# Performance work log

Measured on AMD Instinct MI355X. Metric: run time of the kernel, lower is better.

Reference implementation:

```python
import jax, jax.numpy as jnp
import numpy as np

EMBED_DIM = 1024
NUM_HEADS = 16
HEAD_DIM = EMBED_DIM // NUM_HEADS
B, N = 4, 2048


def setup_inputs() -> dict:
    key = jax.random.key(0)
    k = jax.random.split(key, 5)
    scale = 1.0 / np.sqrt(EMBED_DIM)
    return {
        "x": jax.random.normal(k[0], (B, N, EMBED_DIM), dtype=jnp.float32),
        # torch nn.Linear convention: y = x @ W.T + b, W shape [out, in]
        "qkv_w": jax.random.uniform(k[1], (3 * EMBED_DIM, EMBED_DIM), jnp.float32, -scale, scale),
        "qkv_b": jax.random.uniform(k[2], (3 * EMBED_DIM,), jnp.float32, -scale, scale),
        "out_w": jax.random.uniform(k[3], (EMBED_DIM, EMBED_DIM), jnp.float32, -scale, scale),
        "out_b": jax.random.uniform(k[4], (EMBED_DIM,), jnp.float32, -scale, scale),
    }


def reference(x, qkv_w, qkv_b, out_w, out_b):
    b, n, e = x.shape
    qkv = x @ qkv_w.T + qkv_b                      # [B,N,3E]
    qkv = qkv.reshape(b, n, 3, NUM_HEADS, HEAD_DIM)
    qkv = jnp.transpose(qkv, (2, 0, 3, 1, 4))      # [3,B,H,N,D]
    q, k, v = qkv[0], qkv[1], qkv[2]
    scores = jnp.einsum("bhqd,bhkd->bhqk", q, k) / np.sqrt(HEAD_DIM)
    weights = jax.nn.softmax(scores, axis=-1)
    attn = jnp.einsum("bhqk,bhkd->bhqd", weights, v)  # [B,H,N,D]
    attn = jnp.transpose(attn, (0, 2, 1, 3)).reshape(b, n, e)
    return attn @ out_w.T + out_b
```

## Files before the change

### kernel.cpp

```cpp
#include <hip/hip_runtime.h>
#include <hip/hip_bf16.h>

#define EMBED 1024
#define NHEADS 16
#define HDIM 64
#define BATCH 4
#define SEQ 2048
#define MROWS (BATCH*SEQ)
#define QKVN (3*EMBED)
#define KDIM 1024

typedef __bf16 bf16;
typedef __bf16 bf16x4 __attribute__((ext_vector_type(4)));
typedef __bf16 bf16x8 __attribute__((ext_vector_type(8)));
typedef float f32x4 __attribute__((ext_vector_type(4)));
typedef float f32x16 __attribute__((ext_vector_type(16)));

#define QSCALE 0.18033688011112042f

#define NX (MROWS*EMBED/4)
#define NQ (QKVN*KDIM/4)
#define NO (EMBED*KDIM/4)
__global__ void cvt_all(const float* __restrict__ x, const float* __restrict__ qw,
                        const float* __restrict__ ow,
                        bf16* __restrict__ xb, bf16* __restrict__ qwb, bf16* __restrict__ owb) {
    int i = blockIdx.x * blockDim.x + threadIdx.x;
    const float* src; bf16* dst; int j;
    if (i < NX)            { src = x;  dst = xb;  j = i; }
    else if (i < NX + NQ)  { src = qw; dst = qwb; j = i - NX; }
    else if (i < NX+NQ+NO) { src = ow; dst = owb; j = i - NX - NQ; }
    else return;
    float4 f = ((const float4*)src)[j];
    bf16x4 o;
    o[0] = (bf16)f.x; o[1] = (bf16)f.y; o[2] = (bf16)f.z; o[3] = (bf16)f.w;
    *((bf16x4*)dst + j) = o;
}

template<int MODE>
__launch_bounds__(256)
__global__ void gemm_bt(const bf16* __restrict__ A, const bf16* __restrict__ B,
                        const float* __restrict__ bias,
                        float* __restrict__ outF,
                        bf16* __restrict__ Qb, bf16* __restrict__ Kb, bf16* __restrict__ Vt)
{
    __shared__ __align__(16) char ldsmem[16384];
    bf16 (*Alds)[32] = (bf16(*)[32])ldsmem;
    bf16 (*Blds)[32] = (bf16(*)[32])(ldsmem + 8192);
    bf16* bounce = (bf16*)ldsmem;

    const int tid = threadIdx.x;
    const int l = tid & 63, w = tid >> 6;
    const int wr = w >> 1, wc = w & 1;
    const int tM = blockIdx.y * 128, tN = blockIdx.x * 128;

    f32x4 acc[4][4] = {};
    const bf16* Abase = A + (size_t)tM * KDIM;
    const bf16* Bbase = B + (size_t)tN * KDIM;

    for (int k0 = 0; k0 < KDIM; k0 += 32) {
        #pragma unroll
        for (int t = 0; t < 2; ++t) {
            int idx = t * 256 + tid;
            int row = idx >> 2;
            int kc = (idx & 3) * 8;
            __builtin_amdgcn_global_load_lds(
                (const __attribute__((address_space(1))) void*)(Abase + (size_t)row * KDIM + k0 + kc),
                (__attribute__((address_space(3))) void*)((char*)&Alds[0][0] + idx * 16),
                16, 0, 0);
            __builtin_amdgcn_global_load_lds(
                (const __attribute__((address_space(1))) void*)(Bbase + (size_t)row * KDIM + k0 + kc),
                (__attribute__((address_space(3))) void*)((char*)&Blds[0][0] + idx * 16),
                16, 0, 0);
        }
        __syncthreads();
        bf16x8 a[4], b[4];
        #pragma unroll
        for (int i = 0; i < 4; ++i)
            a[i] = *(const bf16x8*)&Alds[wr * 64 + i * 16 + (l & 15)][(l >> 4) * 8];
        #pragma unroll
        for (int j = 0; j < 4; ++j)
            b[j] = *(const bf16x8*)&Blds[wc * 64 + j * 16 + (l & 15)][(l >> 4) * 8];
        #pragma unroll
        for (int i = 0; i < 4; ++i)
            #pragma unroll
            for (int j = 0; j < 4; ++j)
                acc[i][j] = __builtin_amdgcn_mfma_f32_16x16x32_bf16(a[i], b[j], acc[i][j], 0, 0, 0);
        __syncthreads();
    }

    if (MODE == 1) {
        #pragma unroll
        for (int i = 0; i < 4; ++i) {
            #pragma unroll
            for (int j = 0; j < 4; ++j) {
                int n = tN + wc * 64 + j * 16 + (l & 15);
                float bv = bias[n];
                #pragma unroll
                for (int r = 0; r < 4; ++r) {
                    int m = tM + wr * 64 + i * 16 + (l >> 4) * 4 + r;
                    outF[(size_t)m * EMBED + n] = acc[i][j][r] + bv;
                }
            }
        }
    } else {
        const int which = tN >> 10;
        const int bidx  = tM >> 11;
        const int hd0   = (tN & 1023) >> 6;
        const int t32base = (tM & 2047) >> 5;
        bf16* dstbase = (which == 0) ? Qb : (which == 1) ? Kb : Vt;
        const float scale = (which == 0) ? QSCALE : 1.0f;

        float bj[4];
        #pragma unroll
        for (int j = 0; j < 4; ++j)
            bj[j] = bias[tN + wc * 64 + j * 16 + (l & 15)];

        #pragma unroll
        for (int pass = 0; pass < 2; ++pass) {
            __syncthreads();
            #pragma unroll
            for (int ii = 0; ii < 2; ++ii) {
                const int i = pass * 2 + ii;
                #pragma unroll
                for (int j = 0; j < 4; ++j) {
                    const int d = (wc * 64 + j * 16 + (l & 15)) & 63;
                    #pragma unroll
                    for (int r = 0; r < 4; ++r) {
                        const int nsl = wr * 64 + i * 16 + (l >> 4) * 4 + r;
                        float v = acc[i][j][r] + bj[j];
                        int off;
                        if (which == 2) {
                            int dblk = d >> 5;
                            int rem16 = nsl & 15;
                            int c = (nsl >> 4) & 1;
                            int fj = (rem16 & 3) | ((rem16 & 8) >> 1);
                            int fhi = (rem16 >> 2) & 1;
                            int lane = (d & 31) | (fhi << 5);
                            off = (dblk * 2 + c) * 512 + lane * 8 + fj;
                        } else {
                            int kk = d >> 4, fhi = (d >> 3) & 1, fj = d & 7;
                            int lane = (nsl & 31) | (fhi << 5);
                            off = kk * 512 + lane * 8 + fj;
                        }
                        bounce[(wc * 2 + wr) * 2048 + off] = (bf16)(v * scale);
                    }
                }
            }
            __syncthreads();
            const int chunk = tid >> 6;
            size_t gbase = ((size_t)(bidx * NHEADS + hd0 + (chunk >> 1)) * 64
                            + t32base + 2 * (chunk & 1) + pass) * 2048;
            #pragma unroll
            for (int s = 0; s < 4; ++s) {
                int eoff = s * 512 + (tid & 63) * 8;
                *(bf16x8*)(dstbase + gbase + eoff) = *(const bf16x8*)&bounce[chunk * 2048 + eoff];
            }
        }
    }
}

__launch_bounds__(256)
__global__ void gemm_bt64(const bf16* __restrict__ A, const bf16* __restrict__ B,
                          const float* __restrict__ bias, float* __restrict__ outF)
{
    __shared__ bf16 Alds[64][32];
    __shared__ bf16 Blds[128][32];
    const int tid = threadIdx.x;
    const int l = tid & 63, w = tid >> 6;
    const int tM = blockIdx.y * 64, tN = blockIdx.x * 128;

    f32x4 acc[4][2] = {};
    const bf16* Abase = A + (size_t)tM * KDIM;
    const bf16* Bbase = B + (size_t)tN * KDIM;

    for (int k0 = 0; k0 < KDIM; k0 += 32) {
        {
            int row = tid >> 2;
            int kc = (tid & 3) * 8;
            __builtin_amdgcn_global_load_lds(
                (const __attribute__((address_space(1))) void*)(Abase + (size_t)row * KDIM + k0 + kc),
                (__attribute__((address_space(3))) void*)((char*)&Alds[0][0] + tid * 16),
                16, 0, 0);
        }
        #pragma unroll
        for (int t = 0; t < 2; ++t) {
            int idx = t * 256 + tid;
            int row = idx >> 2;
            int kc = (idx & 3) * 8;
            __builtin_amdgcn_global_load_lds(
                (const __attribute__((address_space(1))) void*)(Bbase + (size_t)row * KDIM + k0 + kc),
                (__attribute__((address_space(3))) void*)((char*)&Blds[0][0] + idx * 16),
                16, 0, 0);
        }
        __syncthreads();
        bf16x8 a[4], b[2];
        #pragma unroll
        for (int i = 0; i < 4; ++i)
            a[i] = *(const bf16x8*)&Alds[i * 16 + (l & 15)][(l >> 4) * 8];
        #pragma unroll
        for (int j = 0; j < 2; ++j)
            b[j] = *(const bf16x8*)&Blds[w * 32 + j * 16 + (l & 15)][(l >> 4) * 8];
        #pragma unroll
        for (int i = 0; i < 4; ++i)
            #pragma unroll
            for (int j = 0; j < 2; ++j)
                acc[i][j] = __builtin_amdgcn_mfma_f32_16x16x32_bf16(a[i], b[j], acc[i][j], 0, 0, 0);
        __syncthreads();
    }

    #pragma unroll
    for (int i = 0; i < 4; ++i) {
        #pragma unroll
        for (int j = 0; j < 2; ++j) {
            int n = tN + w * 32 + j * 16 + (l & 15);
            float bv = bias[n];
            #pragma unroll
            for (int r = 0; r < 4; ++r) {
                int m = tM + i * 16 + (l >> 4) * 4 + r;
                outF[(size_t)m * EMBED + n] = acc[i][j][r] + bv;
            }
        }
    }
}

static __device__ __forceinline__ unsigned cvt_pk(float lo, float hi) {
    unsigned r;
    asm("v_cvt_pk_bf16_f32 %0, %1, %2" : "=v"(r) : "v"(lo), "v"(hi));
    return r;
}

__launch_bounds__(256)
__global__ void attn_kernel(const bf16* __restrict__ Qb, const bf16* __restrict__ Kb,
                            const bf16* __restrict__ Vt, bf16* __restrict__ AO)
{
    const int tid = threadIdx.x, l = tid & 63, w = tid >> 6;
    const int lo5 = l & 31, hi = l >> 5;
    int bid = blockIdx.x;
    int swz = (bid & 7) * 128 + (bid >> 3);
    const int bh = swz >> 4;
    const int qt = swz & 15;

    const bf16* QFh = Qb + (size_t)bh * (64 * 2048);
    const bf16* Kit = Kb + (size_t)bh * (64 * 2048) + (size_t)l * 8;
    const bf16* Vit = Vt + (size_t)bh * (64 * 2048) + (size_t)l * 8;

    const int qtile = qt * 4 + w;
    const bf16* qbase = QFh + (size_t)qtile * 2048 + (size_t)l * 8;
    bf16x8 qf[4];
    #pragma unroll
    for (int kk = 0; kk < 4; ++kk)
        qf[kk] = *(const bf16x8*)(qbase + kk * 512);

    f32x16 O0 = {}, O1 = {};
    float lsum = 0.f;
    const f32x16 ZR = {};

    bf16x8 kK0 = *(const bf16x8*)(Kit);
    bf16x8 kK1 = *(const bf16x8*)(Kit + 512);
    bf16x8 kK2 = *(const bf16x8*)(Kit + 1024);
    bf16x8 kK3 = *(const bf16x8*)(Kit + 1536);
    f32x16 SA, SB;
    SA = __builtin_amdgcn_mfma_f32_32x32x16_bf16(kK0, qf[0], ZR, 0, 0, 0);
    SA = __builtin_amdgcn_mfma_f32_32x32x16_bf16(kK1, qf[1], SA, 0, 0, 0);
    SA = __builtin_amdgcn_mfma_f32_32x32x16_bf16(kK2, qf[2], SA, 0, 0, 0);
    SA = __builtin_amdgcn_mfma_f32_32x32x16_bf16(kK3, qf[3], SA, 0, 0, 0);
    kK0 = *(const bf16x8*)(Kit + 2048);
    kK1 = *(const bf16x8*)(Kit + 2048 + 512);
    kK2 = *(const bf16x8*)(Kit + 2048 + 1024);
    kK3 = *(const bf16x8*)(Kit + 2048 + 1536);

    const bf16* kptr = Kit + 2 * 2048;
    const bf16* vptr = Vit;

#define ATTN_BODY(SCUR, SNXT)                                                            \
    {                                                                                    \
        bf16x8 vf00 = *(const bf16x8*)(vptr);                                            \
        bf16x8 vf01 = *(const bf16x8*)(vptr + 512);                                      \
        bf16x8 vf10 = *(const bf16x8*)(vptr + 1024);                                     \
        bf16x8 vf11 = *(const bf16x8*)(vptr + 1536);                                     \
        vptr += 2048;                                                                    \
        __builtin_amdgcn_s_setprio(1);                                                   \
        SNXT = __builtin_amdgcn_mfma_f32_32x32x16_bf16(kK0, qf[0], ZR, 0, 0, 0);         \
        SNXT = __builtin_amdgcn_mfma_f32_32x32x16_bf16(kK1, qf[1], SNXT, 0, 0, 0);       \
        SNXT = __builtin_amdgcn_mfma_f32_32x32x16_bf16(kK2, qf[2], SNXT, 0, 0, 0);       \
        SNXT = __builtin_amdgcn_mfma_f32_32x32x16_bf16(kK3, qf[3], SNXT, 0, 0, 0);       \
        __builtin_amdgcn_s_setprio(0);                                                   \
        kK0 = *(const bf16x8*)(kptr);                                                    \
        kK1 = *(const bf16x8*)(kptr + 512);                                              \
        kK2 = *(const bf16x8*)(kptr + 1024);                                             \
        kK3 = *(const bf16x8*)(kptr + 1536);                                             \
        kptr += 2048;                                                                    \
        float p[16];                                                                     \
        _Pragma("unroll")                                                                \
        for (int r = 0; r < 16; ++r)                                                     \
            p[r] = __builtin_amdgcn_exp2f(SCUR[r]);                                      \
        float s0 = (p[0] + p[1]) + (p[2] + p[3]);                                        \
        float s1 = (p[4] + p[5]) + (p[6] + p[7]);                                        \
        float s2 = (p[8] + p[9]) + (p[10] + p[11]);                                      \
        float s3 = (p[12] + p[13]) + (p[14] + p[15]);                                    \
        lsum += (s0 + s1) + (s2 + s3);                                                   \
        union { unsigned u[4]; bf16x8 v; } pk0, pk1;                                     \
        pk0.u[0] = cvt_pk(p[0], p[1]);   pk0.u[1] = cvt_pk(p[2], p[3]);                  \
        pk0.u[2] = cvt_pk(p[4], p[5]);   pk0.u[3] = cvt_pk(p[6], p[7]);                  \
        pk1.u[0] = cvt_pk(p[8], p[9]);   pk1.u[1] = cvt_pk(p[10], p[11]);                \
        pk1.u[2] = cvt_pk(p[12], p[13]); pk1.u[3] = cvt_pk(p[14], p[15]);                \
        __builtin_amdgcn_s_setprio(1);                                                   \
        O0 = __builtin_amdgcn_mfma_f32_32x32x16_bf16(vf00, pk0.v, O0, 0, 0, 0);          \
        O0 = __builtin_amdgcn_mfma_f32_32x32x16_bf16(vf01, pk1.v, O0, 0, 0, 0);          \
        O1 = __builtin_amdgcn_mfma_f32_32x32x16_bf16(vf10, pk0.v, O1, 0, 0, 0);          \
        O1 = __builtin_amdgcn_mfma_f32_32x32x16_bf16(vf11, pk1.v, O1, 0, 0, 0);          \
        __builtin_amdgcn_s_setprio(0);                                                   \
    }

    for (int t2 = 0; t2 < 64; t2 += 2) {
        ATTN_BODY(SA, SB)
        ATTN_BODY(SB, SA)
    }
#undef ATTN_BODY

    lsum += __shfl_xor(lsum, 32);
    float linv = 1.0f / lsum;

    const int b = bh >> 4, hd = bh & 15;
    const int q0 = qt * 128 + w * 32;
    bf16* outp = &AO[(size_t)(b * SEQ + q0 + lo5) * EMBED + hd * HDIM];
    #pragma unroll
    for (int g = 0; g < 4; ++g) {
        bf16x4 o0, o1;
        #pragma unroll
        for (int r4 = 0; r4 < 4; ++r4) {
            o0[r4] = (bf16)(O0[g * 4 + r4] * linv);
            o1[r4] = (bf16)(O1[g * 4 + r4] * linv);
        }
        *(bf16x4*)&outp[g * 8 + hi * 4] = o0;
        *(bf16x4*)&outp[32 + g * 8 + hi * 4] = o1;
    }
}

extern "C" void kernel_launch(void* const* d_in, const int* in_sizes, int n_in,
                              void* d_out, int out_size, void* d_ws, size_t ws_size,
                              hipStream_t stream) {
    const float* x     = (const float*)d_in[0];
    const float* qkv_w = (const float*)d_in[1];
    const float* qkv_b = (const float*)d_in[2];
    const float* out_w = (const float*)d_in[3];
    const float* out_b = (const float*)d_in[4];
    float* out = (float*)d_out;

    char* ws = (char*)d_ws;
    bf16* xb  = (bf16*)(ws);
    bf16* qwb = (bf16*)(ws + 16777216);
    bf16* owb = (bf16*)(ws + 23068672);
    bf16* Qb  = (bf16*)(ws + 25165824);
    bf16* Kb  = (bf16*)(ws + 41943040);
    bf16* Vt  = (bf16*)(ws + 58720256);
    bf16* AO  = (bf16*)(ws + 75497472);

    cvt_all<<<(NX + NQ + NO + 255) / 256, 256, 0, stream>>>(x, qkv_w, out_w, xb, qwb, owb);

    gemm_bt<0><<<dim3(QKVN / 128, MROWS / 128), 256, 0, stream>>>(
        xb, qwb, qkv_b, nullptr, Qb, Kb, Vt);

    attn_kernel<<<BATCH * NHEADS * (SEQ / 128), 256, 0, stream>>>(Qb, Kb, Vt, AO);

    gemm_bt64<<<dim3(EMBED / 128, MROWS / 64), 256, 0, stream>>>(AO, owb, out_b, out);
}
```

Baseline: 205.7 us.

## Stage K/V tiles cooperatively into double-buffered LDS via global_load_lds

Each of the four waves previously loaded the full K and V tile for every key block straight from global memory into registers, so each tile was fetched four times. Now each wave asynchronously copies one quarter of the tile into a double-buffered shared-memory array with global_load_lds, and all waves then read the whole tile from LDS. This adds a block barrier on every iteration and drops the old software pipelining, which overlapped the next score MFMA with the current softmax. The launch bounds also gain a min-blocks-per-CU hint of 4. The final prefetch reads one block past the head's K/V data.

```diff
diff --git a/kernel.cpp b/kernel.cpp
--- a/kernel.cpp
+++ b/kernel.cpp
@@ -229,10 +229,11 @@
     return r;
 }
 
-__launch_bounds__(256)
+__launch_bounds__(256, 4)
 __global__ void attn_kernel(const bf16* __restrict__ Qb, const bf16* __restrict__ Kb,
                             const bf16* __restrict__ Vt, bf16* __restrict__ AO)
 {
+    __shared__ bf16 kv[2][2][2048];
     const int tid = threadIdx.x, l = tid & 63, w = tid >> 6;
     const int lo5 = l & 31, hi = l >> 5;
     int bid = blockIdx.x;
@@ -241,8 +242,8 @@
     const int qt = swz & 15;
 
     const bf16* QFh = Qb + (size_t)bh * (64 * 2048);
-    const bf16* Kit = Kb + (size_t)bh * (64 * 2048) + (size_t)l * 8;
-    const bf16* Vit = Vt + (size_t)bh * (64 * 2048) + (size_t)l * 8;
+    const bf16* Ksrc = Kb + (size_t)bh * (64 * 2048) + w * 512 + l * 8;
+    const bf16* Vsrc = Vt + (size_t)bh * (64 * 2048) + w * 512 + l * 8;
 
     const int qtile = qt * 4 + w;
     const bf16* qbase = QFh + (size_t)qtile * 2048 + (size_t)l * 8;
@@ -253,47 +254,43 @@
 
     f32x16 O0 = {}, O1 = {};
     float lsum = 0.f;
-    const f32x16 ZR = {};
-
-    bf16x8 kK0 = *(const bf16x8*)(Kit);
-    bf16x8 kK1 = *(const bf16x8*)(Kit + 512);
-    bf16x8 kK2 = *(const bf16x8*)(Kit + 1024);
-    bf16x8 kK3 = *(const bf16x8*)(Kit + 1536);
-    f32x16 SA, SB;
-    SA = __builtin_amdgcn_mfma_f32_32x32x16_bf16(kK0, qf[0], ZR, 0, 0, 0);
-    SA = __builtin_amdgcn_mfma_f32_32x32x16_bf16(kK1, qf[1], SA, 0, 0, 0);
-    SA = __builtin_amdgcn_mfma_f32_32x32x16_bf16(kK2, qf[2], SA, 0, 0, 0);
-    SA = __builtin_amdgcn_mfma_f32_32x32x16_bf16(kK3, qf[3], SA, 0, 0, 0);
-    kK0 = *(const bf16x8*)(Kit + 2048);
-    kK1 = *(const bf16x8*)(Kit + 2048 + 512);
-    kK2 = *(const bf16x8*)(Kit + 2048 + 1024);
-    kK3 = *(const bf16x8*)(Kit + 2048 + 1536);
-
-    const bf16* kptr = Kit + 2 * 2048;
-    const bf16* vptr = Vit;
-
-#define ATTN_BODY(SCUR, SNXT)                                                            \
+
+#define STAGE(BUF)                                                                       \
     {                                                                                    \
-        bf16x8 vf00 = *(const bf16x8*)(vptr);                                            \
-        bf16x8 vf01 = *(const bf16x8*)(vptr + 512);                                      \
-        bf16x8 vf10 = *(const bf16x8*)(vptr + 1024);                                     \
-        bf16x8 vf11 = *(const bf16x8*)(vptr + 1536);                                     \
-        vptr += 2048;                                                                    \
+        __builtin_amdgcn_global_load_lds(                                                \
+            (const __attribute__((address_space(1))) void*)Ksrc,                         \
+            (__attribute__((address_space(3))) void*)&kv[BUF][0][w * 512], 16, 0, 0);    \
+        __builtin_amdgcn_global_load_lds(                                                \
+            (const __attribute__((address_space(1))) void*)Vsrc,                         \
+            (__attribute__((address_space(3))) void*)&kv[BUF][1][w * 512], 16, 0, 0);    \
+        Ksrc += 2048; Vsrc += 2048;                                                      \
+    }
+
+    STAGE(0)
+    __syncthreads();
+
+#define ATTN_BODY(B)                                                                     \
+    {                                                                                    \
+        STAGE(B ^ 1)                                                                     \
+        bf16x8 kK0 = *(const bf16x8*)&kv[B][0][0 * 512 + l * 8];                         \
+        bf16x8 kK1 = *(const bf16x8*)&kv[B][0][1 * 512 + l * 8];                         \
+        bf16x8 kK2 = *(const bf16x8*)&kv[B][0][2 * 512 + l * 8];                         \
+        bf16x8 kK3 = *(const bf16x8*)&kv[B][0][3 * 512 + l * 8];                         \
+        bf16x8 vf00 = *(const bf16x8*)&kv[B][1][0 * 512 + l * 8];                        \
+        bf16x8 vf01 = *(const bf16x8*)&kv[B][1][1 * 512 + l * 8];                        \
+        bf16x8 vf10 = *(const bf16x8*)&kv[B][1][2 * 512 + l * 8];                        \
+        bf16x8 vf11 = *(const bf16x8*)&kv[B][1][3 * 512 + l * 8];                        \
+        f32x16 S = {};                                                                   \
         __builtin_amdgcn_s_setprio(1);                                                   \
-        SNXT = __builtin_amdgcn_mfma_f32_32x32x16_bf16(kK0, qf[0], ZR, 0, 0, 0);         \
-        SNXT = __builtin_amdgcn_mfma_f32_32x32x16_bf16(kK1, qf[1], SNXT, 0, 0, 0);       \
-        SNXT = __builtin_amdgcn_mfma_f32_32x32x16_bf16(kK2, qf[2], SNXT, 0, 0, 0);       \
-        SNXT = __builtin_amdgcn_mfma_f32_32x32x16_bf16(kK3, qf[3], SNXT, 0, 0, 0);       \
+        S = __builtin_amdgcn_mfma_f32_32x32x16_bf16(kK0, qf[0], S, 0, 0, 0);             \
+        S = __builtin_amdgcn_mfma_f32_32x32x16_bf16(kK1, qf[1], S, 0, 0, 0);             \
+        S = __builtin_amdgcn_mfma_f32_32x32x16_bf16(kK2, qf[2], S, 0, 0, 0);             \
+        S = __builtin_amdgcn_mfma_f32_32x32x16_bf16(kK3, qf[3], S, 0, 0, 0);             \
         __builtin_amdgcn_s_setprio(0);                                                   \
-        kK0 = *(const bf16x8*)(kptr);                                                    \
-        kK1 = *(const bf16x8*)(kptr + 512);                                              \
-        kK2 = *(const bf16x8*)(kptr + 1024);                                             \
-        kK3 = *(const bf16x8*)(kptr + 1536);                                             \
-        kptr += 2048;                                                                    \
         float p[16];                                                                     \
         _Pragma("unroll")                                                                \
         for (int r = 0; r < 16; ++r)                                                     \
-            p[r] = __builtin_amdgcn_exp2f(SCUR[r]);                                      \
+            p[r] = __builtin_amdgcn_exp2f(S[r]);                                         \
         float s0 = (p[0] + p[1]) + (p[2] + p[3]);                                        \
         float s1 = (p[4] + p[5]) + (p[6] + p[7]);                                        \
         float s2 = (p[8] + p[9]) + (p[10] + p[11]);                                      \
@@ -310,13 +307,15 @@
         O1 = __builtin_amdgcn_mfma_f32_32x32x16_bf16(vf10, pk0.v, O1, 0, 0, 0);          \
         O1 = __builtin_amdgcn_mfma_f32_32x32x16_bf16(vf11, pk1.v, O1, 0, 0, 0);          \
         __builtin_amdgcn_s_setprio(0);                                                   \
+        __syncthreads();                                                                 \
     }
 
     for (int t2 = 0; t2 < 64; t2 += 2) {
-        ATTN_BODY(SA, SB)
-        ATTN_BODY(SB, SA)
+        ATTN_BODY(0)
+        ATTN_BODY(1)
     }
 #undef ATTN_BODY
+#undef STAGE
 
     lsum += __shfl_xor(lsum, 32);
     float linv = 1.0f / lsum;
```

After: 191.7 us. -6.8%, faster.
